# Kernel tuning notes

Measured on AMD Instinct MI355X. Metric: run time of the kernel, lower is better.

Reference implementation:

```python
import jax, jax.numpy as jnp
import numpy as np

NS, NC = 16, 8  # n_state, n_ctrl; n_sc = NS + NC


def setup_inputs() -> dict:
    key = jax.random.key(0)
    kQ, kp, kF, kc, kx = jax.random.split(key, 5)
    B, T, nsc = 512, 128, NS + NC
    Qr = jax.random.normal(kQ, (B, T, nsc, nsc), dtype=jnp.float32)
    # PSD + regularized so Quu is invertible (as in the torch example: Q = Q^T Q)
    Q = jnp.einsum('btji,btjk->btik', Qr, Qr) / nsc + jnp.eye(nsc, dtype=jnp.float32)
    p = jax.random.normal(kp, (B, T, nsc), dtype=jnp.float32)
    F = jax.random.normal(kF, (B, T, NS, nsc), dtype=jnp.float32) * 0.3
    c1 = jax.random.normal(kc, (B, T, NS), dtype=jnp.float32)
    x_init = jax.random.normal(kx, (B, NS), dtype=jnp.float32)
    return {"Q": Q, "p": p, "F": F, "c1": c1, "x_init": x_init}


def _lqr(Q, p, F, c1, x_init):
    B, T, nsc = Q.shape[0], Q.shape[1], Q.shape[2]
    ns = F.shape[2]
    # time-major for scan: [T, B, ...]
    Qt = jnp.moveaxis(Q, 1, 0)
    pt = jnp.moveaxis(p, 1, 0)
    Ft = jnp.moveaxis(F, 1, 0)
    ct = jnp.moveaxis(c1, 1, 0)

    def bwd(carry, inp):
        V, v = carry                       # [B,ns,ns], [B,ns]
        Qc, pc, Fc, cc = inp
        # Q_t + F^T V F ; q_t + F^T V c1 + F^T v
        Qh = Qc + jnp.einsum('bni,bnm,bmj->bij', Fc, V, Fc)
        qh = pc + jnp.einsum('bni,bnm,bm->bi', Fc, V, cc) + jnp.einsum('bni,bn->bi', Fc, v)
        Qxx = Qh[:, :ns, :ns]
        Qxu = Qh[:, :ns, ns:]
        Qux = Qh[:, ns:, :ns]
        Quu = Qh[:, ns:, ns:]
        qx = qh[:, :ns]
        qu = qh[:, ns:]
        K = -jnp.linalg.solve(Quu, Qux)                    # [B,nc,ns]
        k = -jnp.linalg.solve(Quu, qu[..., None])[..., 0]  # [B,nc]
        KtQuu = jnp.einsum('bci,bcd->bid', K, Quu)
        Vn = Qxx + Qxu @ K + jnp.einsum('bci,bcj->bij', K, Qux) + KtQuu @ K
        Vn = 0.5 * (Vn + jnp.swapaxes(Vn, -1, -2))
        vn = qx + jnp.einsum('bic,bc->bi', Qxu, k) \
             + jnp.einsum('bci,bc->bi', K, qu) + jnp.einsum('bid,bd->bi', KtQuu, k)
        return (Vn, vn), (K, k)

    V0 = jnp.zeros((B, ns, ns), Q.dtype)
    v0 = jnp.zeros((B, ns), Q.dtype)
    _, (Ks, ks) = jax.lax.scan(bwd, (V0, v0), (Qt, pt, Ft, ct), reverse=True)

    def fwd(x, inp):
        K, k, Fc, cc = inp
        u = jnp.einsum('bci,bi->bc', K, x) + k
        tau = jnp.concatenate([x, u], axis=-1)             # [B, nsc]
        x_next = jnp.einsum('bnj,bj->bn', Fc, tau) + cc
        return x_next, tau

    _, taus = jax.lax.scan(fwd, x_init, (Ks, ks, Ft, ct))
    return jnp.moveaxis(taus, 0, 1)                        # [B, T, nsc]


def reference(Q, p, F, c1, x_init):
    return _lqr(Q, p, F, c1, x_init)
```

## Files before the change

kernel.cpp:

```cpp
#include <hip/hip_runtime.h>

namespace {
constexpr int TT = 128;

__device__ __forceinline__ float rdlane(float v, int l) {
  return __int_as_float(__builtin_amdgcn_readlane(__float_as_int(v), l));
}

__device__ __forceinline__ void bsync() {
  asm volatile("s_waitcnt lgkmcnt(0)" ::: "memory");
  __builtin_amdgcn_s_barrier();
  asm volatile("" ::: "memory");
  __builtin_amdgcn_sched_barrier(0);
}

__global__ __launch_bounds__(256)
void lqr_kernel(const float* __restrict__ Qg, const float* __restrict__ pg,
                const float* __restrict__ Fg, const float* __restrict__ cg,
                const float* __restrict__ x0g, float* __restrict__ out)
{
  __shared__ __align__(16) float VT[16][20];
  __shared__ __align__(16) float vv[16];
  __shared__ __align__(16) float FTxd[2][25][20];
  __shared__ __align__(16) float WTx[25][20];
  __shared__ __align__(16) float QhT[25][36];
  __shared__ __align__(16) float KsT[TT][8][16];
  __shared__ __align__(16) float ksv[TT][8];

  const int tid  = threadIdx.x;
  const int lane = tid & 63;
  const int wv   = tid >> 6;
  const int b    = blockIdx.x;
  const size_t bt0 = (size_t)b * TT;

  const int jl = tid & 31;
  const int g  = tid >> 5;

  for (int e = tid; e < 320; e += 256) (&VT[0][0])[e] = 0.f;
  if (tid < 16) vv[tid] = 0.f;

  const int  fj   = tid >> 2, fk = tid & 3;
  const bool fact = (tid < 100);
  const int  fsw  = (fj < 24) ? ((fj >> 2) & 3) : 2;
  float Fr4[4] = {0.f, 0.f, 0.f, 0.f};

  auto loadF = [&](int t) {
    if (fact) {
      if (fj < 24) {
        const float* Fs = Fg + (bt0 + t) * 384 + fj;
        #pragma unroll
        for (int m = 0; m < 4; ++m) Fr4[m] = Fs[(4 * fk + m) * 24];
      } else {
        const float* cs = cg + (bt0 + t) * 16 + 4 * fk;
        #pragma unroll
        for (int m = 0; m < 4; ++m) Fr4[m] = cs[m];
      }
    }
  };
  auto commitF = [&](int buf) {
    if (fact) {
      float* dst = &FTxd[buf][fj][(fk ^ fsw) << 2];
      *(float4*)dst = make_float4(Fr4[0], Fr4[1], Fr4[2], Fr4[3]);
    }
  };

  float qreg[3] = {0.f, 0.f, 0.f}, qreg3 = 0.f;
  auto loadQ = [&](int t) {
    if (jl < 24) {
      const float* Qs = Qg + (bt0 + t) * 576;
      #pragma unroll
      for (int r = 0; r < 3; ++r) qreg[r] = Qs[(3 * g + r) * 24 + jl];
      if (g == 7) qreg3 = pg[(bt0 + t) * 24 + jl];
    }
  };

  loadF(TT - 1);
  loadQ(TT - 1);
  commitF(1);
  loadF(TT - 2);
  bsync();

  for (int t = TT - 1; t >= 0; --t) {
    const float* Fb = &FTxd[t & 1][0][0];

    float fr[16];
    if (jl < 25) {
      const int sj = (jl >> 2) & 3;
      const float* fb = Fb + jl * 20;
      #pragma unroll
      for (int q = 0; q < 4; ++q) {
        float4 v4 = *(const float4*)(fb + ((q ^ sj) << 2));
        fr[4*q+0] = v4.x; fr[4*q+1] = v4.y; fr[4*q+2] = v4.z; fr[4*q+3] = v4.w;
      }
      const int m0 = 2 * g, m1 = m0 + 1;
      float acc0 = (jl == 24) ? vv[m0] : 0.f;
      float acc1 = (jl == 24) ? vv[m1] : 0.f;
      #pragma unroll
      for (int q = 0; q < 4; ++q) {
        float4 a0 = *(const float4*)(&VT[m0][4*q]);
        float4 a1 = *(const float4*)(&VT[m1][4*q]);
        acc0 = fmaf(a0.x, fr[4*q+0], acc0); acc0 = fmaf(a0.y, fr[4*q+1], acc0);
        acc0 = fmaf(a0.z, fr[4*q+2], acc0); acc0 = fmaf(a0.w, fr[4*q+3], acc0);
        acc1 = fmaf(a1.x, fr[4*q+0], acc1); acc1 = fmaf(a1.y, fr[4*q+1], acc1);
        acc1 = fmaf(a1.z, fr[4*q+2], acc1); acc1 = fmaf(a1.w, fr[4*q+3], acc1);
      }
      float* wb = &WTx[0][0] + jl * 20;
      *(float2*)(wb + ((((g >> 1) ^ sj) << 2) + (m0 & 3))) = make_float2(acc0, acc1);
    }
    bsync();

    if (jl < 24) {
      #pragma unroll
      for (int r = 0; r < 3; ++r) {
        const int c = 3 * g + r;
        const int sc = (c >> 2) & 3;
        const float* wb = &WTx[0][0] + c * 20;
        float acc = qreg[r];
        #pragma unroll
        for (int q = 0; q < 4; ++q) {
          float4 w4 = *(const float4*)(wb + ((q ^ sc) << 2));
          acc = fmaf(w4.x, fr[4*q+0], acc); acc = fmaf(w4.y, fr[4*q+1], acc);
          acc = fmaf(w4.z, fr[4*q+2], acc); acc = fmaf(w4.w, fr[4*q+3], acc);
        }
        float* qb = &QhT[0][0] + c * 36;
        qb[(((jl >> 2) ^ sc) << 2) + (jl & 3)] = acc;
      }
      if (g == 7) {
        const float* wb = &WTx[0][0] + 24 * 20;
        float acc = qreg3;
        #pragma unroll
        for (int q = 0; q < 4; ++q) {
          float4 w4 = *(const float4*)(wb + ((q ^ 2) << 2));
          acc = fmaf(w4.x, fr[4*q+0], acc); acc = fmaf(w4.y, fr[4*q+1], acc);
          acc = fmaf(w4.z, fr[4*q+2], acc); acc = fmaf(w4.w, fr[4*q+3], acc);
        }
        float* qb = &QhT[0][0] + 24 * 36;
        qb[(((jl >> 2) ^ 2) << 2) + (jl & 3)] = acc;
      }
    }
    if (t > 0) loadQ(t - 1);
    bsync();

    if (wv == 2 + (t & 1)) {
      __builtin_amdgcn_s_setprio(1);
      const int cl = (lane < 25) ? lane : 0;
      const int row = (cl < 8) ? (16 + cl) : ((cl < 24) ? (cl - 8) : 24);
      const int s = (row >> 2) & 3;
      const float* base = &QhT[0][0] + row * 36;
      float a_[8];
      {
        float4 x0v = *(const float4*)(base + ((4 ^ s) << 2));
        float4 x1v = *(const float4*)(base + ((5 ^ s) << 2));
        a_[0]=x0v.x; a_[1]=x0v.y; a_[2]=x0v.z; a_[3]=x0v.w;
        a_[4]=x1v.x; a_[5]=x1v.y; a_[6]=x1v.z; a_[7]=x1v.w;
      }
      const int jv = lane & 31;
      const int ih = lane >> 5;
      const int row2 = (jv < 16) ? jv : 24;
      const int s3 = (row2 >> 2) & 3;
      const float* b2 = &QhT[0][0] + row2 * 36;
      const int q0 = 2 * ih, q1 = q0 + 1;
      float4 A0 = *(const float4*)(b2 + ((q0 ^ s3) << 2));
      float4 A1 = *(const float4*)(b2 + ((q1 ^ s3) << 2));
      float4 Bq0[8], Bq1[8];
      #pragma unroll
      for (int c = 0; c < 8; ++c) {
        const int s2 = ((16 + c) >> 2) & 3;
        const float* qb = &QhT[0][0] + (16 + c) * 36;
        Bq0[c] = *(const float4*)(qb + ((q0 ^ s2) << 2));
        Bq1[c] = *(const float4*)(qb + ((q1 ^ s2) << 2));
      }
      #pragma unroll
      for (int pp = 0; pp < 8; ++pp) {
        float f_[8];
        f_[0] = rdlane(a_[0], pp); f_[1] = rdlane(a_[1], pp);
        f_[2] = rdlane(a_[2], pp); f_[3] = rdlane(a_[3], pp);
        f_[4] = rdlane(a_[4], pp); f_[5] = rdlane(a_[5], pp);
        f_[6] = rdlane(a_[6], pp); f_[7] = rdlane(a_[7], pp);
        float d = __builtin_amdgcn_rcpf(f_[pp]);
        a_[pp] *= d;
        #pragma unroll
        for (int r = 0; r < 8; ++r)
          if (r != pp) a_[r] = fmaf(-f_[r], a_[pp], a_[r]);
      }
      if (lane >= 8 && lane < 24) {
        const int j = lane - 8;
        #pragma unroll
        for (int c = 0; c < 8; ++c) KsT[t][c][j] = -a_[c];
      } else if (lane == 24) {
        float4* kp = (float4*)&ksv[t][0];
        kp[0] = make_float4(-a_[0], -a_[1], -a_[2], -a_[3]);
        kp[1] = make_float4(-a_[4], -a_[5], -a_[6], -a_[7]);
      }
      const int sl = (jv < 16) ? (8 + jv) : 24;
      float xj[8];
      #pragma unroll
      for (int c = 0; c < 8; ++c)
        xj[c] = __int_as_float(
            __builtin_amdgcn_ds_bpermute(sl * 4, __float_as_int(a_[c])));
      if (jv < 16 || jv == 24) {
        float acc[8];
        acc[0]=A0.x; acc[1]=A0.y; acc[2]=A0.z; acc[3]=A0.w;
        acc[4]=A1.x; acc[5]=A1.y; acc[6]=A1.z; acc[7]=A1.w;
        #pragma unroll
        for (int c = 0; c < 8; ++c) {
          const float xc = xj[c];
          acc[0] = fmaf(-xc, Bq0[c].x, acc[0]); acc[1] = fmaf(-xc, Bq0[c].y, acc[1]);
          acc[2] = fmaf(-xc, Bq0[c].z, acc[2]); acc[3] = fmaf(-xc, Bq0[c].w, acc[3]);
          acc[4] = fmaf(-xc, Bq1[c].x, acc[4]); acc[5] = fmaf(-xc, Bq1[c].y, acc[5]);
          acc[6] = fmaf(-xc, Bq1[c].z, acc[6]); acc[7] = fmaf(-xc, Bq1[c].w, acc[7]);
        }
        float4* vp = (jv < 16) ? (float4*)&VT[jv][8 * ih] : (float4*)&vv[8 * ih];
        vp[0] = make_float4(acc[0], acc[1], acc[2], acc[3]);
        vp[1] = make_float4(acc[4], acc[5], acc[6], acc[7]);
      }
      __builtin_amdgcn_s_setprio(0);
    } else {
      if (t > 0) commitF((t - 1) & 1);
      if (t > 1) loadF(t - 2);
    }
    bsync();
  }

  if (wv != 0) return;

  float xv = (lane < 16) ? x0g[(size_t)b * 16 + lane] : 0.f;
  float xs_[16];
  #pragma unroll
  for (int i = 0; i < 16; ++i) xs_[i] = rdlane(xv, i);

  float FA[24], FB[24];
  float cA = 0.f, cB = 0.f;
  float KA[16], KB[16], kA = 0.f, kB = 0.f;

  auto loadFw = [&](int t, float (&Fr)[24], float& cr) {
    if (lane < 16) {
      const float* src = Fg + (bt0 + t) * 384 + lane * 24;
      #pragma unroll
      for (int r = 0; r < 6; ++r) {
        float4 f4v = ((const float4*)src)[r];
        Fr[4*r+0] = f4v.x; Fr[4*r+1] = f4v.y; Fr[4*r+2] = f4v.z; Fr[4*r+3] = f4v.w;
      }
      cr = cg[(bt0 + t) * 16 + lane];
    }
  };
  auto loadK = [&](int t, float (&K)[16], float& kk) {
    if (lane < 8) {
      const float4* kp = (const float4*)&KsT[t][lane][0];
      float4 k0 = kp[0], k1 = kp[1], k2 = kp[2], k3 = kp[3];
      K[0]=k0.x;  K[1]=k0.y;  K[2]=k0.z;  K[3]=k0.w;
      K[4]=k1.x;  K[5]=k1.y;  K[6]=k1.z;  K[7]=k1.w;
      K[8]=k2.x;  K[9]=k2.y;  K[10]=k2.z; K[11]=k2.w;
      K[12]=k3.x; K[13]=k3.y; K[14]=k3.z; K[15]=k3.w;
      kk = ksv[t][lane];
    }
  };

  auto fstep = [&](int t, const float (&Fr)[24], float cr,
                   const float (&K)[16], float kk) {
    float uv = 0.f;
    if (lane < 8) {
      float u0 = kk, u1 = 0.f;
      #pragma unroll
      for (int i = 0; i < 16; i += 2) {
        u0 = fmaf(K[i],     xs_[i],     u0);
        u1 = fmaf(K[i + 1], xs_[i + 1], u1);
      }
      uv = u0 + u1;
    }
    float us[8];
    #pragma unroll
    for (int c = 0; c < 8; ++c) us[c] = rdlane(uv, c);
    float* o = out + (bt0 + t) * 24;
    if (lane < 16) o[lane] = xv;
    if (lane < 8)  o[16 + lane] = uv;
    float x0a = cr, x1a = 0.f;
    #pragma unroll
    for (int j2 = 0; j2 < 16; j2 += 2) {
      x0a = fmaf(Fr[j2],     xs_[j2],     x0a);
      x1a = fmaf(Fr[j2 + 1], xs_[j2 + 1], x1a);
    }
    #pragma unroll
    for (int c = 0; c < 8; c += 2) {
      x0a = fmaf(Fr[16 + c],     us[c],     x0a);
      x1a = fmaf(Fr[16 + c + 1], us[c + 1], x1a);
    }
    xv = x0a + x1a;
    #pragma unroll
    for (int i = 0; i < 16; ++i) xs_[i] = rdlane(xv, i);
  };

  loadFw(0, FA, cA); loadK(0, KA, kA);
  for (int t = 0; t < TT; t += 2) {
    if (t + 1 < TT) { loadFw(t + 1, FB, cB); loadK(t + 1, KB, kB); }
    fstep(t, FA, cA, KA, kA);
    if (t + 2 < TT) { loadFw(t + 2, FA, cA); loadK(t + 2, KA, kA); }
    fstep(t + 1, FB, cB, KB, kB);
  }
}
}

extern "C" void kernel_launch(void* const* d_in, const int* in_sizes, int n_in,
                              void* d_out, int out_size, void* d_ws, size_t ws_size,
                              hipStream_t stream)
{
  (void)n_in; (void)out_size; (void)d_ws; (void)ws_size;
  const float* Q  = (const float*)d_in[0];
  const float* p  = (const float*)d_in[1];
  const float* F  = (const float*)d_in[2];
  const float* c1 = (const float*)d_in[3];
  const float* x0 = (const float*)d_in[4];
  float* outp = (float*)d_out;

  const int B = in_sizes[4] / 16;
  lqr_kernel<<<B, 256, 0, stream>>>(Q, p, F, c1, x0, outp);
}
```

Baseline: 258.9 us.

## Partition Qh computation per wave to replace block barrier with wave-local LDS fence

Each wave now owns a set of columns of the F^T V F product, so the intermediate W = V F for those columns is produced and consumed inside the same wave. This lets the block-wide barrier between the two matmul stages become a wave-local lgkmcnt wait. The F operand is re-read from LDS in both stages instead of being held in registers, and the x_init load is hoisted to the kernel start. The cost is more LDS traffic and uneven per-wave work, since wave 0 also handles the p column.

```diff
diff --git a/kernel.cpp b/kernel.cpp
--- a/kernel.cpp
+++ b/kernel.cpp
@@ -11,6 +11,11 @@
   asm volatile("s_waitcnt lgkmcnt(0)" ::: "memory");
   __builtin_amdgcn_s_barrier();
   asm volatile("" ::: "memory");
+  __builtin_amdgcn_sched_barrier(0);
+}
+
+__device__ __forceinline__ void wave_lds_fence() {
+  asm volatile("s_waitcnt lgkmcnt(0)" ::: "memory");
   __builtin_amdgcn_sched_barrier(0);
 }
 
@@ -22,7 +27,7 @@
   __shared__ __align__(16) float VT[16][20];
   __shared__ __align__(16) float vv[16];
   __shared__ __align__(16) float FTxd[2][25][20];
-  __shared__ __align__(16) float WTx[25][20];
+  __shared__ __align__(16) float Wt[25][20];
   __shared__ __align__(16) float QhT[25][36];
   __shared__ __align__(16) float KsT[TT][8][16];
   __shared__ __align__(16) float ksv[TT][8];
@@ -33,11 +38,32 @@
   const int b    = blockIdx.x;
   const size_t bt0 = (size_t)b * TT;
 
-  const int jl = tid & 31;
-  const int g  = tid >> 5;
-
   for (int e = tid; e < 320; e += 256) (&VT[0][0])[e] = 0.f;
   if (tid < 16) vv[tid] = 0.f;
+
+  float xv = 0.f;
+  if (wv == 0 && lane < 16) xv = x0g[(size_t)b * 16 + lane];
+
+  int s1c[2], s1m[2]; bool s1v[2];
+  #pragma unroll
+  for (int k = 0; k < 2; ++k) {
+    const int idx = k * 64 + lane;
+    const int nt  = (wv == 0) ? 112 : 96;
+    s1v[k] = idx < nt;
+    const int cl = idx >> 4;
+    s1c[k] = (wv == 0) ? ((cl == 6) ? 24 : cl) : (6 * wv + cl);
+    s1m[k] = idx & 15;
+  }
+  int s2c[3], s2i[3]; bool s2v[3];
+  #pragma unroll
+  for (int k = 0; k < 3; ++k) {
+    const int idx = k * 64 + lane;
+    const int nt  = (wv == 0) ? 168 : 144;
+    s2v[k] = idx < nt;
+    const int cl = idx / 24;
+    s2c[k] = (wv == 0) ? ((cl == 6) ? 24 : cl) : (6 * wv + cl);
+    s2i[k] = idx - cl * 24;
+  }
 
   const int  fj   = tid >> 2, fk = tid & 3;
   const bool fact = (tid < 100);
@@ -64,13 +90,13 @@
     }
   };
 
-  float qreg[3] = {0.f, 0.f, 0.f}, qreg3 = 0.f;
+  float qreg[3] = {0.f, 0.f, 0.f};
   auto loadQ = [&](int t) {
-    if (jl < 24) {
-      const float* Qs = Qg + (bt0 + t) * 576;
-      #pragma unroll
-      for (int r = 0; r < 3; ++r) qreg[r] = Qs[(3 * g + r) * 24 + jl];
-      if (g == 7) qreg3 = pg[(bt0 + t) * 24 + jl];
+    #pragma unroll
+    for (int k = 0; k < 3; ++k) if (s2v[k]) {
+      qreg[k] = (s2c[k] == 24)
+        ? pg[(bt0 + t) * 24 + s2i[k]]
+        : Qg[(bt0 + t) * 576 + s2c[k] * 24 + s2i[k]];
     }
   };
 
@@ -83,60 +109,39 @@
   for (int t = TT - 1; t >= 0; --t) {
     const float* Fb = &FTxd[t & 1][0][0];
 
-    float fr[16];
-    if (jl < 25) {
-      const int sj = (jl >> 2) & 3;
-      const float* fb = Fb + jl * 20;
+    #pragma unroll
+    for (int k = 0; k < 2; ++k) if (s1v[k]) {
+      const int c = s1c[k], m = s1m[k];
+      const int sj = (c >> 2) & 3;
+      const float* fb = Fb + c * 20;
+      const float* vr = &VT[m][0];
+      float acc = (c == 24) ? vv[m] : 0.f;
       #pragma unroll
       for (int q = 0; q < 4; ++q) {
-        float4 v4 = *(const float4*)(fb + ((q ^ sj) << 2));
-        fr[4*q+0] = v4.x; fr[4*q+1] = v4.y; fr[4*q+2] = v4.z; fr[4*q+3] = v4.w;
-      }
-      const int m0 = 2 * g, m1 = m0 + 1;
-      float acc0 = (jl == 24) ? vv[m0] : 0.f;
-      float acc1 = (jl == 24) ? vv[m1] : 0.f;
+        float4 f4 = *(const float4*)(fb + ((q ^ sj) << 2));
+        float4 v4 = *(const float4*)(vr + 4 * q);
+        acc = fmaf(v4.x, f4.x, acc); acc = fmaf(v4.y, f4.y, acc);
+        acc = fmaf(v4.z, f4.z, acc); acc = fmaf(v4.w, f4.w, acc);
+      }
+      Wt[c][m] = acc;
+    }
+    wave_lds_fence();
+    #pragma unroll
+    for (int k = 0; k < 3; ++k) if (s2v[k]) {
+      const int c = s2c[k], i = s2i[k];
+      const int si = (i >> 2) & 3;
+      const float* fb = Fb + i * 20;
+      const float* wr = &Wt[c][0];
+      float acc = qreg[k];
       #pragma unroll
       for (int q = 0; q < 4; ++q) {
-        float4 a0 = *(const float4*)(&VT[m0][4*q]);
-        float4 a1 = *(const float4*)(&VT[m1][4*q]);
-        acc0 = fmaf(a0.x, fr[4*q+0], acc0); acc0 = fmaf(a0.y, fr[4*q+1], acc0);
-        acc0 = fmaf(a0.z, fr[4*q+2], acc0); acc0 = fmaf(a0.w, fr[4*q+3], acc0);
-        acc1 = fmaf(a1.x, fr[4*q+0], acc1); acc1 = fmaf(a1.y, fr[4*q+1], acc1);
-        acc1 = fmaf(a1.z, fr[4*q+2], acc1); acc1 = fmaf(a1.w, fr[4*q+3], acc1);
-      }
-      float* wb = &WTx[0][0] + jl * 20;
-      *(float2*)(wb + ((((g >> 1) ^ sj) << 2) + (m0 & 3))) = make_float2(acc0, acc1);
-    }
-    bsync();
-
-    if (jl < 24) {
-      #pragma unroll
-      for (int r = 0; r < 3; ++r) {
-        const int c = 3 * g + r;
-        const int sc = (c >> 2) & 3;
-        const float* wb = &WTx[0][0] + c * 20;
-        float acc = qreg[r];
-        #pragma unroll
-        for (int q = 0; q < 4; ++q) {
-          float4 w4 = *(const float4*)(wb + ((q ^ sc) << 2));
-          acc = fmaf(w4.x, fr[4*q+0], acc); acc = fmaf(w4.y, fr[4*q+1], acc);
-          acc = fmaf(w4.z, fr[4*q+2], acc); acc = fmaf(w4.w, fr[4*q+3], acc);
-        }
-        float* qb = &QhT[0][0] + c * 36;
-        qb[(((jl >> 2) ^ sc) << 2) + (jl & 3)] = acc;
-      }
-      if (g == 7) {
-        const float* wb = &WTx[0][0] + 24 * 20;
-        float acc = qreg3;
-        #pragma unroll
-        for (int q = 0; q < 4; ++q) {
-          float4 w4 = *(const float4*)(wb + ((q ^ 2) << 2));
-          acc = fmaf(w4.x, fr[4*q+0], acc); acc = fmaf(w4.y, fr[4*q+1], acc);
-          acc = fmaf(w4.z, fr[4*q+2], acc); acc = fmaf(w4.w, fr[4*q+3], acc);
-        }
-        float* qb = &QhT[0][0] + 24 * 36;
-        qb[(((jl >> 2) ^ 2) << 2) + (jl & 3)] = acc;
-      }
+        float4 f4 = *(const float4*)(fb + ((q ^ si) << 2));
+        float4 w4 = *(const float4*)(wr + 4 * q);
+        acc = fmaf(w4.x, f4.x, acc); acc = fmaf(w4.y, f4.y, acc);
+        acc = fmaf(w4.z, f4.z, acc); acc = fmaf(w4.w, f4.w, acc);
+      }
+      const int sc = (c >> 2) & 3;
+      (&QhT[0][0])[c * 36 + (((i >> 2) ^ sc) << 2) + (i & 3)] = acc;
     }
     if (t > 0) loadQ(t - 1);
     bsync();
@@ -224,7 +229,6 @@
 
   if (wv != 0) return;
 
-  float xv = (lane < 16) ? x0g[(size_t)b * 16 + lane] : 0.f;
   float xs_[16];
   #pragma unroll
   for (int i = 0; i < 16; ++i) xs_[i] = rdlane(xv, i);
```

Measured after the change: 265.6 us. 2.6% more time.

## Double block size to 512 threads and give each thread fewer rows

Applied to the files above, without the earlier changes.

Each block now launches 512 threads instead of 256. The stage computing W = V·F assigns one output per thread instead of two. The stage building Qh assigns one or two rows per thread instead of three or four. The goal is to shorten the serial FMA chain each thread runs inside every step of the time recurrence, which is latency-bound. The x_init load is also moved to the start of the kernel so it is in flight during the backward pass. In exchange, each block-wide barrier now has to synchronise eight waves instead of four, and register pressure per block goes up.

```diff
diff --git a/kernel.cpp b/kernel.cpp
--- a/kernel.cpp
+++ b/kernel.cpp
@@ -14,7 +14,7 @@
   __builtin_amdgcn_sched_barrier(0);
 }
 
-__global__ __launch_bounds__(256)
+__global__ __launch_bounds__(512)
 void lqr_kernel(const float* __restrict__ Qg, const float* __restrict__ pg,
                 const float* __restrict__ Fg, const float* __restrict__ cg,
                 const float* __restrict__ x0g, float* __restrict__ out)
@@ -36,8 +36,11 @@
   const int jl = tid & 31;
   const int g  = tid >> 5;
 
-  for (int e = tid; e < 320; e += 256) (&VT[0][0])[e] = 0.f;
+  if (tid < 320) (&VT[0][0])[tid] = 0.f;
   if (tid < 16) vv[tid] = 0.f;
+
+  float xv = 0.f;
+  if (wv == 0 && lane < 16) xv = x0g[(size_t)b * 16 + lane];
 
   const int  fj   = tid >> 2, fk = tid & 3;
   const bool fact = (tid < 100);
@@ -64,13 +67,12 @@
     }
   };
 
-  float qreg[3] = {0.f, 0.f, 0.f}, qreg3 = 0.f;
+  float qreg0 = 0.f, qreg1 = 0.f;
   auto loadQ = [&](int t) {
     if (jl < 24) {
-      const float* Qs = Qg + (bt0 + t) * 576;
-      #pragma unroll
-      for (int r = 0; r < 3; ++r) qreg[r] = Qs[(3 * g + r) * 24 + jl];
-      if (g == 7) qreg3 = pg[(bt0 + t) * 24 + jl];
+      qreg0 = Qg[(bt0 + t) * 576 + g * 24 + jl];
+      if (g < 8)       qreg1 = Qg[(bt0 + t) * 576 + (16 + g) * 24 + jl];
+      else if (g == 8) qreg1 = pg[(bt0 + t) * 24 + jl];
     }
   };
 
@@ -85,57 +87,53 @@
 
     float fr[16];
     if (jl < 25) {
-      const int sj = (jl >> 2) & 3;
-      const float* fb = Fb + jl * 20;
+      const int c = jl, m = g;
+      const int sj = (c >> 2) & 3;
+      const float* fb = Fb + c * 20;
       #pragma unroll
       for (int q = 0; q < 4; ++q) {
         float4 v4 = *(const float4*)(fb + ((q ^ sj) << 2));
         fr[4*q+0] = v4.x; fr[4*q+1] = v4.y; fr[4*q+2] = v4.z; fr[4*q+3] = v4.w;
       }
-      const int m0 = 2 * g, m1 = m0 + 1;
-      float acc0 = (jl == 24) ? vv[m0] : 0.f;
-      float acc1 = (jl == 24) ? vv[m1] : 0.f;
+      float acc = (c == 24) ? vv[m] : 0.f;
+      const float4* vr4 = (const float4*)&VT[m][0];
       #pragma unroll
       for (int q = 0; q < 4; ++q) {
-        float4 a0 = *(const float4*)(&VT[m0][4*q]);
-        float4 a1 = *(const float4*)(&VT[m1][4*q]);
-        acc0 = fmaf(a0.x, fr[4*q+0], acc0); acc0 = fmaf(a0.y, fr[4*q+1], acc0);
-        acc0 = fmaf(a0.z, fr[4*q+2], acc0); acc0 = fmaf(a0.w, fr[4*q+3], acc0);
-        acc1 = fmaf(a1.x, fr[4*q+0], acc1); acc1 = fmaf(a1.y, fr[4*q+1], acc1);
-        acc1 = fmaf(a1.z, fr[4*q+2], acc1); acc1 = fmaf(a1.w, fr[4*q+3], acc1);
-      }
-      float* wb = &WTx[0][0] + jl * 20;
-      *(float2*)(wb + ((((g >> 1) ^ sj) << 2) + (m0 & 3))) = make_float2(acc0, acc1);
+        float4 v4 = vr4[q];
+        acc = fmaf(v4.x, fr[4*q+0], acc); acc = fmaf(v4.y, fr[4*q+1], acc);
+        acc = fmaf(v4.z, fr[4*q+2], acc); acc = fmaf(v4.w, fr[4*q+3], acc);
+      }
+      float* wb = &WTx[0][0] + c * 20;
+      wb[(((m >> 2) ^ sj) << 2) + (m & 3)] = acc;
     }
     bsync();
 
     if (jl < 24) {
-      #pragma unroll
-      for (int r = 0; r < 3; ++r) {
-        const int c = 3 * g + r;
+      {
+        const int c = g;
         const int sc = (c >> 2) & 3;
         const float* wb = &WTx[0][0] + c * 20;
-        float acc = qreg[r];
+        float acc = qreg0;
         #pragma unroll
         for (int q = 0; q < 4; ++q) {
           float4 w4 = *(const float4*)(wb + ((q ^ sc) << 2));
           acc = fmaf(w4.x, fr[4*q+0], acc); acc = fmaf(w4.y, fr[4*q+1], acc);
           acc = fmaf(w4.z, fr[4*q+2], acc); acc = fmaf(w4.w, fr[4*q+3], acc);
         }
-        float* qb = &QhT[0][0] + c * 36;
-        qb[(((jl >> 2) ^ sc) << 2) + (jl & 3)] = acc;
-      }
-      if (g == 7) {
-        const float* wb = &WTx[0][0] + 24 * 20;
-        float acc = qreg3;
+        (&QhT[0][0])[c * 36 + (((jl >> 2) ^ sc) << 2) + (jl & 3)] = acc;
+      }
+      if (g < 9) {
+        const int c = 16 + g;
+        const int sc = (c >> 2) & 3;
+        const float* wb = &WTx[0][0] + c * 20;
+        float acc = qreg1;
         #pragma unroll
         for (int q = 0; q < 4; ++q) {
-          float4 w4 = *(const float4*)(wb + ((q ^ 2) << 2));
+          float4 w4 = *(const float4*)(wb + ((q ^ sc) << 2));
           acc = fmaf(w4.x, fr[4*q+0], acc); acc = fmaf(w4.y, fr[4*q+1], acc);
           acc = fmaf(w4.z, fr[4*q+2], acc); acc = fmaf(w4.w, fr[4*q+3], acc);
         }
-        float* qb = &QhT[0][0] + 24 * 36;
-        qb[(((jl >> 2) ^ 2) << 2) + (jl & 3)] = acc;
+        (&QhT[0][0])[c * 36 + (((jl >> 2) ^ sc) << 2) + (jl & 3)] = acc;
       }
     }
     if (t > 0) loadQ(t - 1);
@@ -224,7 +222,6 @@
 
   if (wv != 0) return;
 
-  float xv = (lane < 16) ? x0g[(size_t)b * 16 + lane] : 0.f;
   float xs_[16];
   #pragma unroll
   for (int i = 0; i < 16; ++i) xs_[i] = rdlane(xv, i);
@@ -313,5 +310,5 @@
   float* outp = (float*)d_out;
 
   const int B = in_sizes[4] / 16;
-  lqr_kernel<<<B, 256, 0, stream>>>(Q, p, F, c1, x0, outp);
-}
+  lqr_kernel<<<B, 512, 0, stream>>>(Q, p, F, c1, x0, outp);
+}
```

Measured after the change: 399.2 us. 54.2% more time.
